# Kernel tuning notes

Hardware: AMD Instinct MI355X
Metric: run time of the kernel (lower is better)

The kernel has to match this reference:

```python
import jax, jax.numpy as jnp
import numpy as np

B, P, Q, O, H = 2048, 32, 65, 16, 32

def setup_inputs() -> dict:
    key = jax.random.key(0)
    ks = jax.random.split(key, 13)
    s1 = 1.0           # fan_in = 1 for Linear(1,H)
    sH = 1.0 / np.sqrt(H)
    return {
        "x": jax.random.normal(ks[0], (B, P), dtype=jnp.float32),
        # psi_{p,q}: 1 -> H -> H -> 1 MLPs, stacked over (P, Q)
        "psi_w1": jax.random.normal(ks[1], (P, Q, H), dtype=jnp.float32) * s1,
        "psi_b1": jax.random.normal(ks[2], (P, Q, H), dtype=jnp.float32) * s1,
        "psi_w2": jax.random.normal(ks[3], (P, Q, H, H), dtype=jnp.float32) * sH,
        "psi_b2": jax.random.normal(ks[4], (P, Q, H), dtype=jnp.float32) * sH,
        "psi_w3": jax.random.normal(ks[5], (P, Q, H), dtype=jnp.float32) * sH,
        "psi_b3": jax.random.normal(ks[6], (P, Q), dtype=jnp.float32) * sH,
        # phi_{q,i}: 1 -> H -> H -> 1 MLPs, stacked over (Q, O)
        "phi_w1": jax.random.normal(ks[7], (Q, O, H), dtype=jnp.float32) * s1,
        "phi_b1": jax.random.normal(ks[8], (Q, O, H), dtype=jnp.float32) * s1,
        "phi_w2": jax.random.normal(ks[9], (Q, O, H, H), dtype=jnp.float32) * sH,
        "phi_b2": jax.random.normal(ks[10], (Q, O, H), dtype=jnp.float32) * sH,
        "phi_w3": jax.random.normal(ks[11], (Q, O, H), dtype=jnp.float32) * sH,
        "phi_b3": jax.random.normal(ks[12], (Q, O), dtype=jnp.float32) * sH,
    }

def reference(x, psi_w1, psi_b1, psi_w2, psi_b2, psi_w3, psi_b3,
              phi_w1, phi_b1, phi_w2, phi_b2, phi_w3, phi_b3):
    # Inner functions psi_{p,q}(x_p): all P*Q tiny MLPs batched together.
    h = jnp.tanh(x[:, :, None, None] * psi_w1 + psi_b1)                 # [B,P,Q,H]
    h = jnp.tanh(jnp.einsum('bpqh,pqhk->bpqk', h, psi_w2) + psi_b2)     # [B,P,Q,H]
    psi = jnp.einsum('bpqh,pqh->bpq', h, psi_w3) + psi_b3               # [B,P,Q]
    s = psi.sum(axis=1)                                                 # [B,Q]  (sum over p)
    # Outer functions phi_{q,i}(s_q): all Q*O tiny MLPs batched together.
    g = jnp.tanh(s[:, :, None, None] * phi_w1 + phi_b1)                 # [B,Q,O,H]
    g = jnp.tanh(jnp.einsum('bqoh,qohk->bqok', g, phi_w2) + phi_b2)     # [B,Q,O,H]
    phi = jnp.einsum('bqoh,qoh->bqo', g, phi_w3) + phi_b3               # [B,Q,O]
    return phi.sum(axis=1)                                              # [B,O]  (sum over q)
```

## Files before the change

### kernel.cpp

```cpp
#include <hip/hip_runtime.h>

#define B_ 2048
#define P_ 32
#define Q_ 65
#define O_ 16
#define H_ 32

typedef __attribute__((ext_vector_type(8))) short short8;
typedef __attribute__((ext_vector_type(4))) float f32x4;

union F4S8 { float4 f; short8 s; };

#if defined(__has_builtin)
# if __has_builtin(__builtin_amdgcn_exp2f)
#  define HAVE_EXP2 1
# endif
#endif
#ifdef HAVE_EXP2
#define SCALE_K 2.8853900817779268f
__device__ __forceinline__ float exp_z(float y) { return __builtin_amdgcn_exp2f(y); }
#else
#define SCALE_K 2.0f
__device__ __forceinline__ float exp_z(float y) { return __expf(y); }
#endif

__device__ __forceinline__ float tanh_pre(float y) {
    float e = exp_z(y);
    return fmaf(-2.0f, __builtin_amdgcn_rcpf(e + 1.0f), 1.0f);
}

__device__ __forceinline__ unsigned short bf_rne(float f) {
    unsigned u = __float_as_uint(f);
    return (unsigned short)((u + 0x7FFFu + ((u >> 16) & 1u)) >> 16);
}

struct Rec {
    float4 w1a, w1b, b1a, b1b;
    float4 h0, l0, h1, l1;
    float4 ms;
};

template<int MODE>
__device__ __forceinline__ Rec load_rec(
    const float* __restrict__ fragc, const float* __restrict__ shw,
    const float* __restrict__ w1, const float* __restrict__ b1,
    const float* __restrict__ w2, const float* __restrict__ b2,
    const float* __restrict__ w3,
    int pq, int lane, int g, int col)
{
    Rec r;
    if (MODE == 2) {
        const float4* fp = reinterpret_cast<const float4*>(fragc) + (size_t)pq * 256 + lane;
        r.h0 = fp[0]; r.l0 = fp[64]; r.h1 = fp[128]; r.l1 = fp[192];
        const float4* a = reinterpret_cast<const float4*>(shw + (size_t)pq * 128);
        r.w1a = a[g * 2];     r.w1b = a[g * 2 + 1];
        r.b1a = a[8 + g * 2]; r.b1b = a[8 + g * 2 + 1];
        r.ms  = a[16 + col];
    } else {
        const float4* w1p = reinterpret_cast<const float4*>(w1 + pq * H_ + g * 8);
        r.w1a = w1p[0]; r.w1b = w1p[1];
        const float4* b1p = reinterpret_cast<const float4*>(b1 + pq * H_ + g * 8);
        r.b1a = b1p[0]; r.b1b = b1p[1];
        const float* w2p = w2 + (size_t)pq * (H_ * H_);
        F4S8 u0, u1, u2, u3;
        #pragma unroll
        for (int jj = 0; jj < 8; ++jj) {
            float v0 = SCALE_K * w2p[(g * 8 + jj) * H_ + col];
            float v1 = SCALE_K * w2p[(g * 8 + jj) * H_ + 16 + col];
            unsigned q0 = __float_as_uint(v0);
            u0.s[jj] = (short)(q0 >> 16);
            u1.s[jj] = (short)(__float_as_uint(v0 - __uint_as_float(q0 & 0xFFFF0000u)) >> 16);
            unsigned q1 = __float_as_uint(v1);
            u2.s[jj] = (short)(q1 >> 16);
            u3.s[jj] = (short)(__float_as_uint(v1 - __uint_as_float(q1 & 0xFFFF0000u)) >> 16);
        }
        r.h0 = u0.f; r.l0 = u1.f; r.h1 = u2.f; r.l1 = u3.f;
        r.ms = make_float4(SCALE_K * b2[pq * H_ + col], SCALE_K * b2[pq * H_ + 16 + col],
                           w3[pq * H_ + col], w3[pq * H_ + 16 + col]);
    }
    return r;
}

template<bool L1_PRESCALED>
__device__ __forceinline__ void eval_rec(const Rec& r, float xv, float psum[4])
{
    short8 ahi, alo;
#define L1STEP(j, W, Bc)                                                    \
    { float zz = fmaf(xv, (W), (Bc));                                       \
      float y  = L1_PRESCALED ? zz : zz * SCALE_K;                          \
      float tt = tanh_pre(y);                                               \
      unsigned uu = __float_as_uint(tt);                                    \
      ahi[j] = (short)(uu >> 16);                                           \
      float ll = tt - __uint_as_float(uu & 0xFFFF0000u);                    \
      alo[j] = (short)(__float_as_uint(ll) >> 16); }
    L1STEP(0, r.w1a.x, r.b1a.x)
    L1STEP(1, r.w1a.y, r.b1a.y)
    L1STEP(2, r.w1a.z, r.b1a.z)
    L1STEP(3, r.w1a.w, r.b1a.w)
    L1STEP(4, r.w1b.x, r.b1b.x)
    L1STEP(5, r.w1b.y, r.b1b.y)
    L1STEP(6, r.w1b.z, r.b1b.z)
    L1STEP(7, r.w1b.w, r.b1b.w)
#undef L1STEP

    F4S8 c0, c1, c2, c3;
    c0.f = r.h0; c1.f = r.l0; c2.f = r.h1; c3.f = r.l1;
    f32x4 acc0 = {r.ms.x, r.ms.x, r.ms.x, r.ms.x};
    f32x4 acc1 = {r.ms.y, r.ms.y, r.ms.y, r.ms.y};
    acc0 = __builtin_amdgcn_mfma_f32_16x16x32_bf16(ahi, c0.s, acc0, 0, 0, 0);
    acc0 = __builtin_amdgcn_mfma_f32_16x16x32_bf16(alo, c0.s, acc0, 0, 0, 0);
    acc0 = __builtin_amdgcn_mfma_f32_16x16x32_bf16(ahi, c1.s, acc0, 0, 0, 0);
    acc1 = __builtin_amdgcn_mfma_f32_16x16x32_bf16(ahi, c2.s, acc1, 0, 0, 0);
    acc1 = __builtin_amdgcn_mfma_f32_16x16x32_bf16(alo, c2.s, acc1, 0, 0, 0);
    acc1 = __builtin_amdgcn_mfma_f32_16x16x32_bf16(ahi, c3.s, acc1, 0, 0, 0);

    #pragma unroll
    for (int rr = 0; rr < 4; ++rr) {
        psum[rr] = fmaf(tanh_pre(acc0[rr]), r.ms.z, psum[rr]);
        psum[rr] = fmaf(tanh_pre(acc1[rr]), r.ms.w, psum[rr]);
    }
}

__device__ __forceinline__ void reduce_store(float psum[4], float b3sum,
                                             int lane, int g, int b0w,
                                             float* addr_base, int stride, bool atomic)
{
    #pragma unroll
    for (int rr = 0; rr < 4; ++rr) {
        psum[rr] += __shfl_xor(psum[rr], 1);
        psum[rr] += __shfl_xor(psum[rr], 2);
        psum[rr] += __shfl_xor(psum[rr], 4);
        psum[rr] += __shfl_xor(psum[rr], 8);
    }
    float v01 = (lane & 1) ? psum[1] : psum[0];
    float v23 = (lane & 1) ? psum[3] : psum[2];
    float v = (lane & 2) ? v23 : v01;
    if ((lane & 15) < 4) {
        int row = b0w + g * 4 + (lane & 3);
        float* a = addr_base + (size_t)row * stride;
        if (atomic) atomicAdd(a, v + b3sum);
        else        *a = v + b3sum;
    }
}

template<int MODE>
__global__ __launch_bounds__(256)
void psi_main(const float* __restrict__ x, const float* __restrict__ xT,
              const float* __restrict__ w1, const float* __restrict__ b1,
              const float* __restrict__ w2, const float* __restrict__ b2,
              const float* __restrict__ w3, const float* __restrict__ b3,
              const float* __restrict__ b3c,
              const float* __restrict__ fragc, const float* __restrict__ shw,
              float* __restrict__ sT)
{
    const int id = blockIdx.x;
    const int j = (id & 7) * 260 + (id >> 3);
    const int q = j >> 5;
    const int btile = j & 31;
    const int lane = threadIdx.x & 63;
    const int wid = threadIdx.x >> 6;
    const int g = lane >> 4, col = lane & 15;
    const int b0w = btile * 64 + wid * 16;

    float psum[4] = {0.f, 0.f, 0.f, 0.f};
    float b3sum = (MODE == 2) ? b3c[q] : 0.f;

    Rec cur = load_rec<MODE>(fragc, shw, w1, b1, w2, b2, w3, q, lane, g, col);
    float xv = (MODE == 2) ? xT[b0w + col] : x[(size_t)(b0w + col) * P_];

    #pragma unroll 2
    for (int p = 0; p < P_; ++p) {
        const int pn = (p + 1 < P_) ? p + 1 : P_ - 1;
        Rec nxt = load_rec<MODE>(fragc, shw, w1, b1, w2, b2, w3,
                                 pn * Q_ + q, lane, g, col);
        float xn = (MODE == 2) ? xT[(size_t)pn * B_ + b0w + col]
                               : x[(size_t)(b0w + col) * P_ + pn];
        if (MODE != 2) b3sum += b3[p * Q_ + q];
        eval_rec<(MODE == 2)>(cur, xv, psum);
        cur = nxt; xv = xn;
    }

    reduce_store(psum, b3sum, lane, g, b0w, sT + (size_t)q * B_, 1, false);
}

template<int MODE>
__global__ __launch_bounds__(256)
void phi_main(const float* __restrict__ sT,
              const float* __restrict__ w1, const float* __restrict__ b1,
              const float* __restrict__ w2, const float* __restrict__ b2,
              const float* __restrict__ w3, const float* __restrict__ b3,
              const float* __restrict__ b3g,
              const float* __restrict__ fragc, const float* __restrict__ shw,
              float* __restrict__ out)
{
    const int id = blockIdx.x;
    const int j = (id & 7) * 320 + (id >> 3);
    const int qg = j >> 9;
    const int rem = j & 511;
    const int o = rem >> 5;
    const int btile = rem & 31;
    const int lane = threadIdx.x & 63;
    const int wid = threadIdx.x >> 6;
    const int g = lane >> 4, col = lane & 15;
    const int b0w = btile * 64 + wid * 16;

    float psum[4] = {0.f, 0.f, 0.f, 0.f};
    float b3sum = (MODE == 2) ? b3g[qg * O_ + o] : 0.f;

    const int q0 = qg * 13;
    Rec cur = load_rec<MODE>(fragc, shw, w1, b1, w2, b2, w3, q0 * O_ + o, lane, g, col);
    float sv = sT[(size_t)q0 * B_ + b0w + col];

    #pragma unroll 2
    for (int i = 0; i < 13; ++i) {
        const int in_ = (i + 1 < 13) ? i + 1 : 12;
        const int qn = q0 + in_;
        Rec nxt = load_rec<MODE>(fragc, shw, w1, b1, w2, b2, w3,
                                 qn * O_ + o, lane, g, col);
        float sn = sT[(size_t)qn * B_ + b0w + col];
        if (MODE != 2) b3sum += b3[(q0 + i) * O_ + o];
        eval_rec<(MODE == 2)>(cur, sv, psum);
        cur = nxt; sv = sn;
    }

    reduce_store(psum, b3sum, lane, g, b0w, out + o, O_, true);
}

__device__ __forceinline__ void do_frag(const float* __restrict__ w2,
                                        float* __restrict__ frag, int idx)
{
    int pq = idx >> 6, lane = idx & 63;
    int g = lane >> 4, col = lane & 15;
    const float* Wp = w2 + (size_t)pq * (H_ * H_);
    short8 h0v, l0v, h1v, l1v;
    #pragma unroll
    for (int jj = 0; jj < 8; ++jj) {
        float v0 = SCALE_K * Wp[(g * 8 + jj) * H_ + col];
        float v1 = SCALE_K * Wp[(g * 8 + jj) * H_ + 16 + col];
        unsigned short hb0 = bf_rne(v0);
        h0v[jj] = (short)hb0;
        l0v[jj] = (short)bf_rne(v0 - __uint_as_float(((unsigned)hb0) << 16));
        unsigned short hb1 = bf_rne(v1);
        h1v[jj] = (short)hb1;
        l1v[jj] = (short)bf_rne(v1 - __uint_as_float(((unsigned)hb1) << 16));
    }
    F4S8 a, b, c, d; a.s = h0v; b.s = l0v; c.s = h1v; d.s = l1v;
    float4* op = reinterpret_cast<float4*>(frag) + (size_t)pq * 256 + lane;
    op[0] = a.f; op[64] = b.f; op[128] = c.f; op[192] = d.f;
}

__device__ __forceinline__ void do_shw(const float* __restrict__ w1,
                                       const float* __restrict__ b1,
                                       const float* __restrict__ b2,
                                       const float* __restrict__ w3,
                                       float* __restrict__ shw, int idx)
{
    int pq = idx >> 7, i = idx & 127;
    float v;
    if (i < 32)       v = SCALE_K * w1[pq * H_ + i];
    else if (i < 64)  v = SCALE_K * b1[pq * H_ + (i - 32)];
    else {
        int c = (i - 64) >> 2, rr = i & 3;
        v = (rr == 0) ? SCALE_K * b2[pq * H_ + c]
          : (rr == 1) ? SCALE_K * b2[pq * H_ + c + 16]
          : (rr == 2) ? w3[pq * H_ + c]
          :             w3[pq * H_ + c + 16];
    }
    shw[(size_t)pq * 128 + i] = v;
}

#define N1 133120
#define N2 66560
#define N3 266240
#define N4 133120
#define N5 65536
#define C1 133120
#define C2 199680
#define C3 465920
#define C4 599040
#define C5 664576
#define C6 664641
#define C7 664721

__global__ __launch_bounds__(256)
void prep_all(const float* __restrict__ psi_w1, const float* __restrict__ psi_b1,
              const float* __restrict__ psi_w2, const float* __restrict__ psi_b2,
              const float* __restrict__ psi_w3, const float* __restrict__ psi_b3,
              const float* __restrict__ phi_w1, const float* __restrict__ phi_b1,
              const float* __restrict__ phi_w2, const float* __restrict__ phi_b2,
              const float* __restrict__ phi_w3, const float* __restrict__ phi_b3,
              const float* __restrict__ x,
              float* __restrict__ fr1, float* __restrict__ fr2,
              float* __restrict__ sh1, float* __restrict__ sh2,
              float* __restrict__ xT, float* __restrict__ b3c,
              float* __restrict__ b3g)
{
    int t = blockIdx.x * 256 + threadIdx.x;
    if (t < C1) {
        do_frag(psi_w2, fr1, t);
    } else if (t < C2) {
        do_frag(phi_w2, fr2, t - C1);
    } else if (t < C3) {
        do_shw(psi_w1, psi_b1, psi_b2, psi_w3, sh1, t - C2);
    } else if (t < C4) {
        do_shw(phi_w1, phi_b1, phi_b2, phi_w3, sh2, t - C3);
    } else if (t < C5) {
        int idx = t - C4;
        int b = idx >> 5, p = idx & 31;
        xT[(size_t)p * B_ + b] = x[idx];
    } else if (t < C6) {
        int q = t - C5;
        float s = 0.f;
        for (int p = 0; p < P_; ++p) s += psi_b3[p * Q_ + q];
        b3c[q] = s;
    } else if (t < C7) {
        int idx = t - C6;
        int qg = idx >> 4, o = idx & 15;
        float s = 0.f;
        for (int i = 0; i < 13; ++i) s += phi_b3[(qg * 13 + i) * O_ + o];
        b3g[idx] = s;
    }
}

extern "C" void kernel_launch(void* const* d_in, const int* in_sizes, int n_in,
                              void* d_out, int out_size, void* d_ws, size_t ws_size,
                              hipStream_t stream) {
    const float* x      = (const float*)d_in[0];
    const float* psi_w1 = (const float*)d_in[1];
    const float* psi_b1 = (const float*)d_in[2];
    const float* psi_w2 = (const float*)d_in[3];
    const float* psi_b2 = (const float*)d_in[4];
    const float* psi_w3 = (const float*)d_in[5];
    const float* psi_b3 = (const float*)d_in[6];
    const float* phi_w1 = (const float*)d_in[7];
    const float* phi_b1 = (const float*)d_in[8];
    const float* phi_w2 = (const float*)d_in[9];
    const float* phi_b2 = (const float*)d_in[10];
    const float* phi_w3 = (const float*)d_in[11];
    const float* phi_b3 = (const float*)d_in[12];
    float* out = (float*)d_out;

    const size_t ST  = (size_t)B_ * Q_ * sizeof(float);
    const size_t XT  = (size_t)B_ * P_ * sizeof(float);
    const size_t FR1 = (size_t)N1 * 64;
    const size_t FR2 = (size_t)N2 * 64;
    const size_t SH1 = (size_t)N3 * 4;
    const size_t SH2 = (size_t)N4 * 4;
    const size_t B3C = 320;
    const size_t B3G = 320;

    float* sT = (float*)d_ws;
    hipMemsetAsync(out, 0, (size_t)B_ * O_ * sizeof(float), stream);

    if (ws_size >= ST + XT + FR1 + FR2 + SH1 + SH2 + B3C + B3G) {
        char* base = (char*)d_ws + ST;
        float* xTp  = (float*)base;                   base += XT;
        float* fr1  = (float*)base;                   base += FR1;
        float* fr2  = (float*)base;                   base += FR2;
        float* sh1  = (float*)base;                   base += SH1;
        float* sh2  = (float*)base;                   base += SH2;
        float* b3c  = (float*)base;                   base += B3C;
        float* b3g  = (float*)base;

        prep_all<<<(C7 + 255) / 256, 256, 0, stream>>>(
            psi_w1, psi_b1, psi_w2, psi_b2, psi_w3, psi_b3,
            phi_w1, phi_b1, phi_w2, phi_b2, phi_w3, phi_b3,
            x, fr1, fr2, sh1, sh2, xTp, b3c, b3g);

        psi_main<2><<<2080, 256, 0, stream>>>(
            x, xTp, psi_w1, psi_b1, psi_w2, psi_b2, psi_w3, psi_b3, b3c,
            fr1, sh1, sT);
        phi_main<2><<<2560, 256, 0, stream>>>(
            sT, phi_w1, phi_b1, phi_w2, phi_b2, phi_w3, phi_b3, b3g,
            fr2, sh2, out);
    } else {
        psi_main<0><<<2080, 256, 0, stream>>>(
            x, x, psi_w1, psi_b1, psi_w2, psi_b2, psi_w3, psi_b3, (const float*)sT,
            sT, sT, sT);
        phi_main<0><<<2560, 256, 0, stream>>>(
            sT, phi_w1, phi_b1, phi_w2, phi_b2, phi_w3, phi_b3, (const float*)sT,
            sT, sT, out);
    }
}
```

Measured before the change: 220.3 us.

## Fold tanh affine terms into weights and rebalance phi q-groups to 2048 blocks

Tanh is rewritten as 1 - 2*sigmoid-complement, and the affine parts are folded into precomputed weights. W2 is scaled by -2, b2 absorbs the column sums of W2, w3 is scaled by -2, and b3 absorbs the sums of w3, so each activation needs only exp, add and rcp. The hi/lo bf16 split now uses packed hardware conversion instead of manual truncation. The phi kernel regroups Q into four groups (17,16,16,16) instead of five groups of 13, which lowers the grid to 2048 blocks, and prep computes the extra folded sums. Rounding-to-nearest on the split and the folded constants change numerics slightly.

New measurement: 247.8 us. +12.5%, slower.

```diff
diff --git a/kernel.cpp b/kernel.cpp
--- a/kernel.cpp
+++ b/kernel.cpp
@@ -1,4 +1,5 @@
 #include <hip/hip_runtime.h>
+#include <hip/hip_bf16.h>
 
 #define B_ 2048
 #define P_ 32
@@ -9,7 +10,7 @@
 typedef __attribute__((ext_vector_type(8))) short short8;
 typedef __attribute__((ext_vector_type(4))) float f32x4;
 
-union F4S8 { float4 f; short8 s; };
+union F4S8 { float4 f; short8 s; unsigned u[4]; };
 
 #if defined(__has_builtin)
 # if __has_builtin(__builtin_amdgcn_exp2f)
@@ -24,14 +25,18 @@
 __device__ __forceinline__ float exp_z(float y) { return __expf(y); }
 #endif
 
-__device__ __forceinline__ float tanh_pre(float y) {
-    float e = exp_z(y);
-    return fmaf(-2.0f, __builtin_amdgcn_rcpf(e + 1.0f), 1.0f);
+__device__ __forceinline__ float sigc(float y) {
+    return __builtin_amdgcn_rcpf(exp_z(y) + 1.0f);
 }
 
 __device__ __forceinline__ unsigned short bf_rne(float f) {
     unsigned u = __float_as_uint(f);
     return (unsigned short)((u + 0x7FFFu + ((u >> 16) & 1u)) >> 16);
+}
+
+__device__ __forceinline__ unsigned pk_bf16(float a, float b) {
+    __hip_bfloat162 h = __float22bfloat162_rn(make_float2(a, b));
+    return *reinterpret_cast<unsigned*>(&h);
 }
 
 struct Rec {
@@ -63,10 +68,11 @@
         r.b1a = b1p[0]; r.b1b = b1p[1];
         const float* w2p = w2 + (size_t)pq * (H_ * H_);
         F4S8 u0, u1, u2, u3;
+        float cs0 = 0.f, cs1 = 0.f;
         #pragma unroll
         for (int jj = 0; jj < 8; ++jj) {
-            float v0 = SCALE_K * w2p[(g * 8 + jj) * H_ + col];
-            float v1 = SCALE_K * w2p[(g * 8 + jj) * H_ + 16 + col];
+            float v0 = -2.f * SCALE_K * w2p[(g * 8 + jj) * H_ + col];
+            float v1 = -2.f * SCALE_K * w2p[(g * 8 + jj) * H_ + 16 + col];
             unsigned q0 = __float_as_uint(v0);
             u0.s[jj] = (short)(q0 >> 16);
             u1.s[jj] = (short)(__float_as_uint(v0 - __uint_as_float(q0 & 0xFFFF0000u)) >> 16);
@@ -74,50 +80,60 @@
             u2.s[jj] = (short)(q1 >> 16);
             u3.s[jj] = (short)(__float_as_uint(v1 - __uint_as_float(q1 & 0xFFFF0000u)) >> 16);
         }
+        for (int h = 0; h < H_; ++h) {
+            cs0 += w2p[h * H_ + col];
+            cs1 += w2p[h * H_ + 16 + col];
+        }
         r.h0 = u0.f; r.l0 = u1.f; r.h1 = u2.f; r.l1 = u3.f;
-        r.ms = make_float4(SCALE_K * b2[pq * H_ + col], SCALE_K * b2[pq * H_ + 16 + col],
-                           w3[pq * H_ + col], w3[pq * H_ + 16 + col]);
+        r.ms = make_float4(SCALE_K * (b2[pq * H_ + col] + cs0),
+                           SCALE_K * (b2[pq * H_ + 16 + col] + cs1),
+                           -2.f * w3[pq * H_ + col],
+                           -2.f * w3[pq * H_ + 16 + col]);
     }
     return r;
 }
 
-template<bool L1_PRESCALED>
+template<bool PRE>
 __device__ __forceinline__ void eval_rec(const Rec& r, float xv, float psum[4])
 {
-    short8 ahi, alo;
-#define L1STEP(j, W, Bc)                                                    \
-    { float zz = fmaf(xv, (W), (Bc));                                       \
-      float y  = L1_PRESCALED ? zz : zz * SCALE_K;                          \
-      float tt = tanh_pre(y);                                               \
-      unsigned uu = __float_as_uint(tt);                                    \
-      ahi[j] = (short)(uu >> 16);                                           \
-      float ll = tt - __uint_as_float(uu & 0xFFFF0000u);                    \
-      alo[j] = (short)(__float_as_uint(ll) >> 16); }
-    L1STEP(0, r.w1a.x, r.b1a.x)
-    L1STEP(1, r.w1a.y, r.b1a.y)
-    L1STEP(2, r.w1a.z, r.b1a.z)
-    L1STEP(3, r.w1a.w, r.b1a.w)
-    L1STEP(4, r.w1b.x, r.b1b.x)
-    L1STEP(5, r.w1b.y, r.b1b.y)
-    L1STEP(6, r.w1b.z, r.b1b.z)
-    L1STEP(7, r.w1b.w, r.b1b.w)
-#undef L1STEP
+    float s0 = sigc(PRE ? fmaf(xv, r.w1a.x, r.b1a.x) : SCALE_K * fmaf(xv, r.w1a.x, r.b1a.x));
+    float s1 = sigc(PRE ? fmaf(xv, r.w1a.y, r.b1a.y) : SCALE_K * fmaf(xv, r.w1a.y, r.b1a.y));
+    float s2 = sigc(PRE ? fmaf(xv, r.w1a.z, r.b1a.z) : SCALE_K * fmaf(xv, r.w1a.z, r.b1a.z));
+    float s3 = sigc(PRE ? fmaf(xv, r.w1a.w, r.b1a.w) : SCALE_K * fmaf(xv, r.w1a.w, r.b1a.w));
+    float s4 = sigc(PRE ? fmaf(xv, r.w1b.x, r.b1b.x) : SCALE_K * fmaf(xv, r.w1b.x, r.b1b.x));
+    float s5 = sigc(PRE ? fmaf(xv, r.w1b.y, r.b1b.y) : SCALE_K * fmaf(xv, r.w1b.y, r.b1b.y));
+    float s6 = sigc(PRE ? fmaf(xv, r.w1b.z, r.b1b.z) : SCALE_K * fmaf(xv, r.w1b.z, r.b1b.z));
+    float s7 = sigc(PRE ? fmaf(xv, r.w1b.w, r.b1b.w) : SCALE_K * fmaf(xv, r.w1b.w, r.b1b.w));
+
+    F4S8 hi, lo;
+    hi.u[0] = pk_bf16(s0, s1); hi.u[1] = pk_bf16(s2, s3);
+    hi.u[2] = pk_bf16(s4, s5); hi.u[3] = pk_bf16(s6, s7);
+    float l0v = s0 - __uint_as_float(hi.u[0] << 16);
+    float l1v = s1 - __uint_as_float(hi.u[0] & 0xFFFF0000u);
+    float l2v = s2 - __uint_as_float(hi.u[1] << 16);
+    float l3v = s3 - __uint_as_float(hi.u[1] & 0xFFFF0000u);
+    float l4v = s4 - __uint_as_float(hi.u[2] << 16);
+    float l5v = s5 - __uint_as_float(hi.u[2] & 0xFFFF0000u);
+    float l6v = s6 - __uint_as_float(hi.u[3] << 16);
+    float l7v = s7 - __uint_as_float(hi.u[3] & 0xFFFF0000u);
+    lo.u[0] = pk_bf16(l0v, l1v); lo.u[1] = pk_bf16(l2v, l3v);
+    lo.u[2] = pk_bf16(l4v, l5v); lo.u[3] = pk_bf16(l6v, l7v);
 
     F4S8 c0, c1, c2, c3;
     c0.f = r.h0; c1.f = r.l0; c2.f = r.h1; c3.f = r.l1;
     f32x4 acc0 = {r.ms.x, r.ms.x, r.ms.x, r.ms.x};
     f32x4 acc1 = {r.ms.y, r.ms.y, r.ms.y, r.ms.y};
-    acc0 = __builtin_amdgcn_mfma_f32_16x16x32_bf16(ahi, c0.s, acc0, 0, 0, 0);
-    acc0 = __builtin_amdgcn_mfma_f32_16x16x32_bf16(alo, c0.s, acc0, 0, 0, 0);
-    acc0 = __builtin_amdgcn_mfma_f32_16x16x32_bf16(ahi, c1.s, acc0, 0, 0, 0);
-    acc1 = __builtin_amdgcn_mfma_f32_16x16x32_bf16(ahi, c2.s, acc1, 0, 0, 0);
-    acc1 = __builtin_amdgcn_mfma_f32_16x16x32_bf16(alo, c2.s, acc1, 0, 0, 0);
-    acc1 = __builtin_amdgcn_mfma_f32_16x16x32_bf16(ahi, c3.s, acc1, 0, 0, 0);
+    acc0 = __builtin_amdgcn_mfma_f32_16x16x32_bf16(hi.s, c0.s, acc0, 0, 0, 0);
+    acc0 = __builtin_amdgcn_mfma_f32_16x16x32_bf16(lo.s, c0.s, acc0, 0, 0, 0);
+    acc0 = __builtin_amdgcn_mfma_f32_16x16x32_bf16(hi.s, c1.s, acc0, 0, 0, 0);
+    acc1 = __builtin_amdgcn_mfma_f32_16x16x32_bf16(hi.s, c2.s, acc1, 0, 0, 0);
+    acc1 = __builtin_amdgcn_mfma_f32_16x16x32_bf16(lo.s, c2.s, acc1, 0, 0, 0);
+    acc1 = __builtin_amdgcn_mfma_f32_16x16x32_bf16(hi.s, c3.s, acc1, 0, 0, 0);
 
     #pragma unroll
     for (int rr = 0; rr < 4; ++rr) {
-        psum[rr] = fmaf(tanh_pre(acc0[rr]), r.ms.z, psum[rr]);
-        psum[rr] = fmaf(tanh_pre(acc1[rr]), r.ms.w, psum[rr]);
+        psum[rr] = fmaf(sigc(acc0[rr]), r.ms.z, psum[rr]);
+        psum[rr] = fmaf(sigc(acc1[rr]), r.ms.w, psum[rr]);
     }
 }
 
@@ -175,7 +191,11 @@
                                  pn * Q_ + q, lane, g, col);
         float xn = (MODE == 2) ? xT[(size_t)pn * B_ + b0w + col]
                                : x[(size_t)(b0w + col) * P_ + pn];
-        if (MODE != 2) b3sum += b3[p * Q_ + q];
+        if (MODE != 2) {
+            float ws = 0.f;
+            for (int h = 0; h < H_; ++h) ws += w3[(p * Q_ + q) * H_ + h];
+            b3sum += b3[p * Q_ + q] + ws;
+        }
         eval_rec<(MODE == 2)>(cur, xv, psum);
         cur = nxt; xv = xn;
     }
@@ -194,7 +214,7 @@
               float* __restrict__ out)
 {
     const int id = blockIdx.x;
-    const int j = (id & 7) * 320 + (id >> 3);
+    const int j = (id & 7) * 256 + (id >> 3);
     const int qg = j >> 9;
     const int rem = j & 511;
     const int o = rem >> 5;
@@ -204,21 +224,27 @@
     const int g = lane >> 4, col = lane & 15;
     const int b0w = btile * 64 + wid * 16;
 
+    const int q0  = (qg == 0) ? 0 : 17 + (qg - 1) * 16;
+    const int len = (qg == 0) ? 17 : 16;
+
     float psum[4] = {0.f, 0.f, 0.f, 0.f};
     float b3sum = (MODE == 2) ? b3g[qg * O_ + o] : 0.f;
 
-    const int q0 = qg * 13;
     Rec cur = load_rec<MODE>(fragc, shw, w1, b1, w2, b2, w3, q0 * O_ + o, lane, g, col);
     float sv = sT[(size_t)q0 * B_ + b0w + col];
 
     #pragma unroll 2
-    for (int i = 0; i < 13; ++i) {
-        const int in_ = (i + 1 < 13) ? i + 1 : 12;
+    for (int i = 0; i < len; ++i) {
+        const int in_ = (i + 1 < len) ? i + 1 : len - 1;
         const int qn = q0 + in_;
         Rec nxt = load_rec<MODE>(fragc, shw, w1, b1, w2, b2, w3,
                                  qn * O_ + o, lane, g, col);
         float sn = sT[(size_t)qn * B_ + b0w + col];
-        if (MODE != 2) b3sum += b3[(q0 + i) * O_ + o];
+        if (MODE != 2) {
+            float ws = 0.f;
+            for (int h = 0; h < H_; ++h) ws += w3[((q0 + i) * O_ + o) * H_ + h];
+            b3sum += b3[(q0 + i) * O_ + o] + ws;
+        }
         eval_rec<(MODE == 2)>(cur, sv, psum);
         cur = nxt; sv = sn;
     }
@@ -235,8 +261,8 @@
     short8 h0v, l0v, h1v, l1v;
     #pragma unroll
     for (int jj = 0; jj < 8; ++jj) {
-        float v0 = SCALE_K * Wp[(g * 8 + jj) * H_ + col];
-        float v1 = SCALE_K * Wp[(g * 8 + jj) * H_ + 16 + col];
+        float v0 = -2.f * SCALE_K * Wp[(g * 8 + jj) * H_ + col];
+        float v1 = -2.f * SCALE_K * Wp[(g * 8 + jj) * H_ + 16 + col];
         unsigned short hb0 = bf_rne(v0);
         h0v[jj] = (short)hb0;
         l0v[jj] = (short)bf_rne(v0 - __uint_as_float(((unsigned)hb0) << 16));
@@ -251,6 +277,7 @@
 
 __device__ __forceinline__ void do_shw(const float* __restrict__ w1,
                                        const float* __restrict__ b1,
+                                       const float* __restrict__ w2,
                                        const float* __restrict__ b2,
                                        const float* __restrict__ w3,
                                        float* __restrict__ shw, int idx)
@@ -261,26 +288,27 @@
     else if (i < 64)  v = SCALE_K * b1[pq * H_ + (i - 32)];
     else {
         int c = (i - 64) >> 2, rr = i & 3;
-        v = (rr == 0) ? SCALE_K * b2[pq * H_ + c]
-          : (rr == 1) ? SCALE_K * b2[pq * H_ + c + 16]
-          : (rr == 2) ? w3[pq * H_ + c]
-          :             w3[pq * H_ + c + 16];
+        if (rr <= 1) {
+            int cc = c + (rr == 1 ? 16 : 0);
+            float cs = 0.f;
+            const float* Wp = w2 + (size_t)pq * (H_ * H_);
+            for (int h = 0; h < H_; ++h) cs += Wp[h * H_ + cc];
+            v = SCALE_K * (b2[pq * H_ + cc] + cs);
+        } else {
+            int cc = c + (rr == 3 ? 16 : 0);
+            v = -2.f * w3[pq * H_ + cc];
+        }
     }
     shw[(size_t)pq * 128 + i] = v;
 }
 
-#define N1 133120
-#define N2 66560
-#define N3 266240
-#define N4 133120
-#define N5 65536
 #define C1 133120
 #define C2 199680
 #define C3 465920
 #define C4 599040
 #define C5 664576
 #define C6 664641
-#define C7 664721
+#define C7 664705
 
 __global__ __launch_bounds__(256)
 void prep_all(const float* __restrict__ psi_w1, const float* __restrict__ psi_b1,
@@ -301,9 +329,9 @@
     } else if (t < C2) {
         do_frag(phi_w2, fr2, t - C1);
     } else if (t < C3) {
-        do_shw(psi_w1, psi_b1, psi_b2, psi_w3, sh1, t - C2);
+        do_shw(psi_w1, psi_b1, psi_w2, psi_b2, psi_w3, sh1, t - C2);
     } else if (t < C4) {
-        do_shw(phi_w1, phi_b1, phi_b2, phi_w3, sh2, t - C3);
+        do_shw(phi_w1, phi_b1, phi_w2, phi_b2, phi_w3, sh2, t - C3);
     } else if (t < C5) {
         int idx = t - C4;
         int b = idx >> 5, p = idx & 31;
@@ -311,13 +339,23 @@
     } else if (t < C6) {
         int q = t - C5;
         float s = 0.f;
-        for (int p = 0; p < P_; ++p) s += psi_b3[p * Q_ + q];
+        for (int p = 0; p < P_; ++p) {
+            int pq = p * Q_ + q;
+            s += psi_b3[pq];
+            for (int h = 0; h < H_; ++h) s += psi_w3[pq * H_ + h];
+        }
         b3c[q] = s;
     } else if (t < C7) {
         int idx = t - C6;
         int qg = idx >> 4, o = idx & 15;
+        int q0  = (qg == 0) ? 0 : 17 + (qg - 1) * 16;
+        int len = (qg == 0) ? 17 : 16;
         float s = 0.f;
-        for (int i = 0; i < 13; ++i) s += phi_b3[(qg * 13 + i) * O_ + o];
+        for (int i = 0; i < len; ++i) {
+            int qo = (q0 + i) * O_ + o;
+            s += phi_b3[qo];
+            for (int h = 0; h < H_; ++h) s += phi_w3[qo * H_ + h];
+        }
         b3g[idx] = s;
     }
 }
@@ -342,10 +380,10 @@
 
     const size_t ST  = (size_t)B_ * Q_ * sizeof(float);
     const size_t XT  = (size_t)B_ * P_ * sizeof(float);
-    const size_t FR1 = (size_t)N1 * 64;
-    const size_t FR2 = (size_t)N2 * 64;
-    const size_t SH1 = (size_t)N3 * 4;
-    const size_t SH2 = (size_t)N4 * 4;
+    const size_t FR1 = (size_t)P_ * Q_ * 64 * 64;
+    const size_t FR2 = (size_t)Q_ * O_ * 64 * 64;
+    const size_t SH1 = (size_t)P_ * Q_ * 128 * 4;
+    const size_t SH2 = (size_t)Q_ * O_ * 128 * 4;
     const size_t B3C = 320;
     const size_t B3G = 320;
 
@@ -370,14 +408,14 @@
         psi_main<2><<<2080, 256, 0, stream>>>(
             x, xTp, psi_w1, psi_b1, psi_w2, psi_b2, psi_w3, psi_b3, b3c,
             fr1, sh1, sT);
-        phi_main<2><<<2560, 256, 0, stream>>>(
+        phi_main<2><<<2048, 256, 0, stream>>>(
             sT, phi_w1, phi_b1, phi_w2, phi_b2, phi_w3, phi_b3, b3g,
             fr2, sh2, out);
     } else {
         psi_main<0><<<2080, 256, 0, stream>>>(
             x, x, psi_w1, psi_b1, psi_w2, psi_b2, psi_w3, psi_b3, (const float*)sT,
             sT, sT, sT);
-        phi_main<0><<<2560, 256, 0, stream>>>(
+        phi_main<0><<<2048, 256, 0, stream>>>(
             sT, phi_w1, phi_b1, phi_w2, phi_b2, phi_w3, phi_b3, (const float*)sT,
             sT, sT, out);
     }
```
